# Kernel tuning notes

Measured on AMD Instinct MI355X. Metric: run time of the kernel, lower is better.

Reference implementation:

```python
import jax, jax.numpy as jnp
import numpy as np

N_NODES = 50000


def _gcn_layer(x, src, dst, norm_src, norm_dst, W, b, act):
    # DGL GraphConv with norm='both': D_out^{-1/2} A D_in^{-1/2} X W + b
    h = x * norm_src[:, None]                      # scale by src out-degree
    m = h[src]                                     # gather messages [E, d]
    agg = jax.ops.segment_sum(m, dst, num_segments=N_NODES)  # scatter-add
    agg = agg * norm_dst[:, None]
    out = agg @ W + b
    if act:
        out = jax.nn.relu(out)
    return out


def setup_inputs() -> dict:
    key = jax.random.key(0)
    ks = jax.random.split(key, 10)
    E = 800000
    in_size, hid, out_size = 128, 128, 64
    features = jax.random.normal(ks[0], (N_NODES, in_size), dtype=jnp.float32)
    src = jax.random.randint(ks[1], (E,), 0, N_NODES, dtype=jnp.int32)
    dst = jax.random.randint(ks[2], (E,), 0, N_NODES, dtype=jnp.int32)
    s = 0.05
    W1 = jax.random.normal(ks[3], (in_size, hid), dtype=jnp.float32) * s
    b1 = jnp.zeros((hid,), dtype=jnp.float32)
    W2 = jax.random.normal(ks[4], (hid, hid), dtype=jnp.float32) * s
    b2 = jnp.zeros((hid,), dtype=jnp.float32)
    W3 = jax.random.normal(ks[5], (hid, out_size), dtype=jnp.float32) * s
    b3 = jnp.zeros((out_size,), dtype=jnp.float32)
    return {"features": features, "W1": W1, "b1": b1, "W2": W2, "b2": b2,
            "W3": W3, "b3": b3, "src": src, "dst": dst}


def reference(features, W1, b1, W2, b2, W3, b3, src, dst):
    ones = jnp.ones(src.shape, dtype=features.dtype)
    out_deg = jax.ops.segment_sum(ones, src, num_segments=N_NODES)
    in_deg = jax.ops.segment_sum(ones, dst, num_segments=N_NODES)
    norm_src = jnp.maximum(out_deg, 1.0) ** -0.5   # clamp(min=1) as in DGL
    norm_dst = jnp.maximum(in_deg, 1.0) ** -0.5
    h = _gcn_layer(features, src, dst, norm_src, norm_dst, W1, b1, act=True)
    # dropout is identity in eval mode
    h = _gcn_layer(h, src, dst, norm_src, norm_dst, W2, b2, act=True)
    h = _gcn_layer(h, src, dst, norm_src, norm_dst, W3, b3, act=False)
    return h
```

## Files before the change

kernel.cpp:

```cpp
#include <hip/hip_runtime.h>
#include <math.h>

#define N_NODES 50000
#define K_DIM 128
#define CAP 64
#define CHUNK 25000
#define RH 25000
#define HWORDS 12500

typedef __attribute__((ext_vector_type(8))) short short8_t;
typedef __attribute__((ext_vector_type(4))) float f32x4_t;
typedef __attribute__((ext_vector_type(8))) _Float16 half8_t;

__device__ inline unsigned short f2bf(float x) {
    unsigned u = __float_as_uint(x);
    unsigned r = u + 0x7fffu + ((u >> 16) & 1u);
    return (unsigned short)(r >> 16);
}
__device__ inline float bf2f(unsigned short h) {
    return __uint_as_float(((unsigned)h) << 16);
}

__global__ void init_zero_kernel(_Float16* Yx, _Float16* Yy, _Float16* Yz) {
    int t = threadIdx.x;
    if (t < 128) {
        Yx[(size_t)N_NODES * 128 + t] = (_Float16)0.f;
        Yy[(size_t)N_NODES * 128 + t] = (_Float16)0.f;
    }
    if (t < 64) Yz[(size_t)N_NODES * 64 + t] = (_Float16)0.f;
}


__global__ __launch_bounds__(1024) void hist_kernel(const int* __restrict__ src,
                                                    const int* __restrict__ dst, int E,
                                                    unsigned* __restrict__ pin,
                                                    unsigned* __restrict__ pout) {
    __shared__ unsigned h[HWORDS];
    int b  = blockIdx.x >> 2;
    int io = (blockIdx.x >> 1) & 1;
    int r  = blockIdx.x & 1;
    int tid = threadIdx.x;
    for (int t = tid; t < HWORDS; t += 1024) h[t] = 0;
    __syncthreads();
    const int* keys = io ? src : dst;
    int start = b * CHUNK;
    int end = start + CHUNK; if (end > E) end = E;
    int vlo = r * RH;
    for (int i = start + tid; i < end; i += 1024) {
        int v = keys[i] - vlo;
        if ((unsigned)v < (unsigned)RH)
            atomicAdd(&h[v >> 1], 1u << ((v & 1) * 16));
    }
    __syncthreads();
    unsigned* out = io ? pout : pin;
    for (int t = tid; t < HWORDS; t += 1024)
        out[(size_t)b * (2 * HWORDS) + r * HWORDS + t] = h[t];
}

__global__ void offsets_norm_kernel(const unsigned* __restrict__ pin,
                                    const unsigned* __restrict__ pout,
                                    unsigned short* __restrict__ off16,
                                    int* __restrict__ indeg,
                                    float* __restrict__ nsrc, float* __restrict__ ndst,
                                    int n, int NB) {
    int v = blockIdx.x * blockDim.x + threadIdx.x;
    if (v >= n) return;
    int wi = v >> 1, sh = (v & 1) * 16;
    int od = 0;
    for (int b = 0; b < NB; ++b)
        od += (pout[(size_t)b * (2 * HWORDS) + wi] >> sh) & 0xffff;
    int run = 0;
    for (int b = 0; b < NB; ++b) {
        int c = (pin[(size_t)b * (2 * HWORDS) + wi] >> sh) & 0xffff;
        off16[(size_t)b * n + v] = (unsigned short)(run < CAP ? run : CAP);
        run += c;
    }
    indeg[v] = run < CAP ? run : CAP;
    int odc = od < 1 ? 1 : od;
    int idc = run < 1 ? 1 : run;
    nsrc[v] = 1.0f / sqrtf((float)odc);
    ndst[v] = 1.0f / sqrtf((float)idc);
}

__global__ __launch_bounds__(1024) void scatter_kernel(const int* __restrict__ src,
                                                       const int* __restrict__ dst, int E,
                                                       const unsigned short* __restrict__ off16,
                                                       int* __restrict__ csr, int n) {
    __shared__ unsigned cur[HWORDS];
    int b = blockIdx.x >> 1;
    int r = blockIdx.x & 1;
    int tid = threadIdx.x;
    int vlo = r * RH;
    const unsigned short* offb = off16 + (size_t)b * n + vlo;
    for (int t = tid; t < HWORDS; t += 1024)
        cur[t] = (unsigned)offb[2 * t] | ((unsigned)offb[2 * t + 1] << 16);
    __syncthreads();
    int start = b * CHUNK;
    int end = start + CHUNK; if (end > E) end = E;
    for (int i = start + tid; i < end; i += 1024) {
        int v = dst[i];
        int vr = v - vlo;
        if ((unsigned)vr < (unsigned)RH) {
            int sh = (vr & 1) * 16;
            unsigned old = atomicAdd(&cur[vr >> 1], 1u << sh);
            unsigned p = (old >> sh) & 0xffff;
            if (p < CAP) csr[((size_t)v << 6) + p] = src[i];
        }
    }
}

__global__ void split_w_all_kernel(const float* __restrict__ W1,
                                   const float* __restrict__ W2,
                                   const float* __restrict__ W3,
                                   unsigned short* __restrict__ W1h, unsigned short* __restrict__ W1l,
                                   unsigned short* __restrict__ W2h, unsigned short* __restrict__ W2l,
                                   unsigned short* __restrict__ W3h, unsigned short* __restrict__ W3l) {
    int gi = blockIdx.x * blockDim.x + threadIdx.x;
    const float* W; unsigned short *WBh, *WBl; int M, i;
    if (gi < 2048)      { W = W1; WBh = W1h; WBl = W1l; M = 128; i = gi; }
    else if (gi < 4096) { W = W2; WBh = W2h; WBl = W2l; M = 128; i = gi - 2048; }
    else if (gi < 5120) { W = W3; WBh = W3h; WBl = W3l; M = 64;  i = gi - 4096; }
    else return;
    int c    = i >> 8;
    int rem  = i & 255;
    int kc   = rem >> 6;
    int lane = rem & 63;
    int m = lane & 15, q = lane >> 4;
    int n = c * 16 + m;
    #pragma unroll
    for (int j = 0; j < 8; ++j) {
        int k = kc * 32 + q * 8 + j;
        float w = W[(size_t)k * M + n];
        unsigned short hi = f2bf(w);
        unsigned short lo = f2bf(w - bf2f(hi));
        WBh[(size_t)i * 8 + j] = hi;
        WBl[(size_t)i * 8 + j] = lo;
    }
}

template <int M>
__global__ __launch_bounds__(256) void gemm_mfma_kernel(
        const float* __restrict__ X,
        const unsigned short* __restrict__ WBh_,
        const unsigned short* __restrict__ WBl_,
        const float* __restrict__ nsrc, _Float16* __restrict__ Yh, int n) {
    constexpr int LSTR = 136;
    __shared__ short Xhi[64 * LSTR];
    __shared__ short Xlo[64 * LSTR];
    int tid = threadIdx.x;
    int lane = tid & 63, wave = tid >> 6;
    int rowBlock = blockIdx.x * 64;

    #pragma unroll
    for (int l = 0; l < 8; ++l) {
        int idx = (tid + l * 256) * 4;
        int r = idx >> 7;
        int c = idx & 127;
        float4 v = make_float4(0.f, 0.f, 0.f, 0.f);
        int gr = rowBlock + r;
        if (gr < n) v = *(const float4*)&X[(size_t)gr * K_DIM + c];
        unsigned short h0 = f2bf(v.x), h1 = f2bf(v.y), h2 = f2bf(v.z), h3 = f2bf(v.w);
        short4 hs = {(short)h0, (short)h1, (short)h2, (short)h3};
        short4 ls = {(short)f2bf(v.x - bf2f(h0)), (short)f2bf(v.y - bf2f(h1)),
                     (short)f2bf(v.z - bf2f(h2)), (short)f2bf(v.w - bf2f(h3))};
        *(short4*)&Xhi[r * LSTR + c] = hs;
        *(short4*)&Xlo[r * LSTR + c] = ls;
    }
    __syncthreads();

    int m = lane & 15, q = lane >> 4;
    short8_t ah[4], al[4];
    {
        int abase = (wave * 16 + m) * LSTR + q * 8;
        #pragma unroll
        for (int kc = 0; kc < 4; ++kc) {
            ah[kc] = *(const short8_t*)&Xhi[abase + kc * 32];
            al[kc] = *(const short8_t*)&Xlo[abase + kc * 32];
        }
    }
    float ns[4];
    int orow0 = rowBlock + wave * 16 + q * 4;
    #pragma unroll
    for (int r = 0; r < 4; ++r) ns[r] = (orow0 + r < n) ? nsrc[orow0 + r] : 0.f;

    const short8_t* WBh = (const short8_t*)WBh_;
    const short8_t* WBl = (const short8_t*)WBl_;
    constexpr int CT = M / 16;
    #pragma unroll
    for (int c = 0; c < CT; ++c) {
        short8_t bh[4], bl[4];
        #pragma unroll
        for (int kc = 0; kc < 4; ++kc) {
            bh[kc] = WBh[(c * 4 + kc) * 64 + lane];
            bl[kc] = WBl[(c * 4 + kc) * 64 + lane];
        }
        f32x4_t acc = {0.f, 0.f, 0.f, 0.f};
        #pragma unroll
        for (int kc = 0; kc < 4; ++kc) {
            acc = __builtin_amdgcn_mfma_f32_16x16x32_bf16(ah[kc], bh[kc], acc, 0, 0, 0);
            acc = __builtin_amdgcn_mfma_f32_16x16x32_bf16(ah[kc], bl[kc], acc, 0, 0, 0);
            acc = __builtin_amdgcn_mfma_f32_16x16x32_bf16(al[kc], bh[kc], acc, 0, 0, 0);
        }
        int col = c * 16 + m;
        #pragma unroll
        for (int r = 0; r < 4; ++r) {
            int row = orow0 + r;
            if (row < n) Yh[(size_t)row * M + col] = (_Float16)(acc[r] * ns[r]);
        }
    }
}

template <int MOUT>
__global__ __launch_bounds__(256) void agg_gemm_kernel(
        const _Float16* __restrict__ Yin,
        const int* __restrict__ indeg, const int* __restrict__ csr,
        const float* __restrict__ ndst, const float* __restrict__ bias,
        const unsigned short* __restrict__ WBh_,
        const unsigned short* __restrict__ WBl_,
        const float* __restrict__ nsrc, _Float16* __restrict__ Yout, int n) {
    constexpr int LSTR = 136;
    __shared__ short Xhi[64 * LSTR];
    __shared__ short Xlo[64 * LSTR];
    int tid = threadIdx.x;
    int lane = tid & 63, wave = tid >> 6;
    int rowBlock = blockIdx.x * 64;

    int sub = tid >> 4;
    int f8  = (tid & 15) * 8;
    #pragma unroll
    for (int p = 0; p < 4; ++p) {
        int r = p * 16 + sub;
        int v = rowBlock + r;
        float o[8] = {};
        if (v < n) {
            int deg = indeg[v];
            const int* __restrict__ row = &csr[(size_t)v * CAP];
            float acc[8] = {};
            for (int i = 0; i < deg; i += 4) {
                int4 ss = *(const int4*)&row[i];
                int s0 = ss.x;
                int s1 = (i + 1 < deg) ? ss.y : N_NODES;
                int s2 = (i + 2 < deg) ? ss.z : N_NODES;
                int s3 = (i + 3 < deg) ? ss.w : N_NODES;
                half8_t a = *(const half8_t*)&Yin[(size_t)s0 * 128 + f8];
                half8_t b = *(const half8_t*)&Yin[(size_t)s1 * 128 + f8];
                half8_t c = *(const half8_t*)&Yin[(size_t)s2 * 128 + f8];
                half8_t d = *(const half8_t*)&Yin[(size_t)s3 * 128 + f8];
                #pragma unroll
                for (int j = 0; j < 8; ++j)
                    acc[j] += ((float)a[j] + (float)b[j]) + ((float)c[j] + (float)d[j]);
            }
            float nd = ndst[v];
            #pragma unroll
            for (int j = 0; j < 8; ++j)
                o[j] = fmaxf(nd * acc[j] + bias[f8 + j], 0.f);
        }
        short hs[8], ls[8];
        #pragma unroll
        for (int j = 0; j < 8; ++j) {
            unsigned short h = f2bf(o[j]);
            hs[j] = (short)h;
            ls[j] = (short)f2bf(o[j] - bf2f(h));
        }
        *(short4*)&Xhi[r * LSTR + f8]     = *(short4*)&hs[0];
        *(short4*)&Xhi[r * LSTR + f8 + 4] = *(short4*)&hs[4];
        *(short4*)&Xlo[r * LSTR + f8]     = *(short4*)&ls[0];
        *(short4*)&Xlo[r * LSTR + f8 + 4] = *(short4*)&ls[4];
    }
    __syncthreads();

    int m = lane & 15, q = lane >> 4;
    short8_t ah[4], al[4];
    {
        int abase = (wave * 16 + m) * LSTR + q * 8;
        #pragma unroll
        for (int kc = 0; kc < 4; ++kc) {
            ah[kc] = *(const short8_t*)&Xhi[abase + kc * 32];
            al[kc] = *(const short8_t*)&Xlo[abase + kc * 32];
        }
    }
    float ns[4];
    int orow0 = rowBlock + wave * 16 + q * 4;
    #pragma unroll
    for (int r = 0; r < 4; ++r) ns[r] = (orow0 + r < n) ? nsrc[orow0 + r] : 0.f;

    const short8_t* WBh = (const short8_t*)WBh_;
    const short8_t* WBl = (const short8_t*)WBl_;
    constexpr int CT = MOUT / 16;
    #pragma unroll
    for (int c = 0; c < CT; ++c) {
        short8_t bh[4], bl[4];
        #pragma unroll
        for (int kc = 0; kc < 4; ++kc) {
            bh[kc] = WBh[(c * 4 + kc) * 64 + lane];
            bl[kc] = WBl[(c * 4 + kc) * 64 + lane];
        }
        f32x4_t acc = {0.f, 0.f, 0.f, 0.f};
        #pragma unroll
        for (int kc = 0; kc < 4; ++kc) {
            acc = __builtin_amdgcn_mfma_f32_16x16x32_bf16(ah[kc], bh[kc], acc, 0, 0, 0);
            acc = __builtin_amdgcn_mfma_f32_16x16x32_bf16(ah[kc], bl[kc], acc, 0, 0, 0);
            acc = __builtin_amdgcn_mfma_f32_16x16x32_bf16(al[kc], bh[kc], acc, 0, 0, 0);
        }
        int col = c * 16 + m;
        #pragma unroll
        for (int r = 0; r < 4; ++r) {
            int row = orow0 + r;
            if (row < n) Yout[(size_t)row * MOUT + col] = (_Float16)(acc[r] * ns[r]);
        }
    }
}

template <int M, bool RELU>
__global__ __launch_bounds__(256) void agg_kernel(const _Float16* __restrict__ Y,
                                                  const int* __restrict__ indeg,
                                                  const int* __restrict__ csr,
                                                  const float* __restrict__ ndst,
                                                  const float* __restrict__ bias,
                                                  float* __restrict__ Z, int n) {
    constexpr int LPN = M / 8;
    constexpr int NPB = 256 / LPN;
    int v = blockIdx.x * NPB + threadIdx.x / LPN;
    if (v >= n) return;
    int f8 = (threadIdx.x % LPN) * 8;
    int deg = indeg[v];
    const int* __restrict__ row = &csr[(size_t)v * CAP];
    float acc[8] = {};
    for (int i = 0; i < deg; i += 4) {
        int4 ss = *(const int4*)&row[i];
        int s0 = ss.x;
        int s1 = (i + 1 < deg) ? ss.y : N_NODES;
        int s2 = (i + 2 < deg) ? ss.z : N_NODES;
        int s3 = (i + 3 < deg) ? ss.w : N_NODES;
        half8_t a = *(const half8_t*)&Y[(size_t)s0 * M + f8];
        half8_t b = *(const half8_t*)&Y[(size_t)s1 * M + f8];
        half8_t c = *(const half8_t*)&Y[(size_t)s2 * M + f8];
        half8_t d = *(const half8_t*)&Y[(size_t)s3 * M + f8];
        #pragma unroll
        for (int j = 0; j < 8; ++j)
            acc[j] += ((float)a[j] + (float)b[j]) + ((float)c[j] + (float)d[j]);
    }
    float nd = ndst[v];
    float4 bb0 = *(const float4*)&bias[f8];
    float4 bb1 = *(const float4*)&bias[f8 + 4];
    float o[8];
    o[0] = nd * acc[0] + bb0.x; o[1] = nd * acc[1] + bb0.y;
    o[2] = nd * acc[2] + bb0.z; o[3] = nd * acc[3] + bb0.w;
    o[4] = nd * acc[4] + bb1.x; o[5] = nd * acc[5] + bb1.y;
    o[6] = nd * acc[6] + bb1.z; o[7] = nd * acc[7] + bb1.w;
    if (RELU) {
        #pragma unroll
        for (int j = 0; j < 8; ++j) o[j] = fmaxf(o[j], 0.f);
    }
    *(float4*)&Z[(size_t)v * M + f8]     = make_float4(o[0], o[1], o[2], o[3]);
    *(float4*)&Z[(size_t)v * M + f8 + 4] = make_float4(o[4], o[5], o[6], o[7]);
}


extern "C" void kernel_launch(void* const* d_in, const int* in_sizes, int n_in,
                              void* d_out, int out_size, void* d_ws, size_t ws_size,
                              hipStream_t stream) {
    const float* features = (const float*)d_in[0];
    const float* W1 = (const float*)d_in[1];
    const float* b1 = (const float*)d_in[2];
    const float* W2 = (const float*)d_in[3];
    const float* b2 = (const float*)d_in[4];
    const float* W3 = (const float*)d_in[5];
    const float* b3 = (const float*)d_in[6];
    const int* src = (const int*)d_in[7];
    const int* dst = (const int*)d_in[8];
    const int E = in_sizes[7];
    const int N = N_NODES;
    const int NB = (E + CHUNK - 1) / CHUNK;

    char* w = (char*)d_ws;
    auto alloc = [&](size_t bytes) {
        char* p = w;
        w += (bytes + 255) & ~(size_t)255;
        return p;
    };
    _Float16* Yx = (_Float16*)alloc((size_t)(N + 1) * 128 * 2);
    _Float16* Yy = (_Float16*)alloc((size_t)(N + 1) * 128 * 2);
    _Float16* Yz = (_Float16*)alloc((size_t)(N + 1) * 64 * 2);
    int*   csr    = (int*)alloc((size_t)N * CAP * 4);
    unsigned* pin  = (unsigned*)alloc((size_t)NB * 2 * HWORDS * 4);
    unsigned* pout = (unsigned*)alloc((size_t)NB * 2 * HWORDS * 4);
    unsigned short* off16 = (unsigned short*)alloc((size_t)NB * N * 2);
    int*   indeg  = (int*)alloc((size_t)N * 4);
    float* nsrc   = (float*)alloc((size_t)N * 4);
    float* ndst   = (float*)alloc((size_t)N * 4);
    unsigned short* W1h = (unsigned short*)alloc(128 * 128 * 2);
    unsigned short* W1l = (unsigned short*)alloc(128 * 128 * 2);
    unsigned short* W2h = (unsigned short*)alloc(128 * 128 * 2);
    unsigned short* W2l = (unsigned short*)alloc(128 * 128 * 2);
    unsigned short* W3h = (unsigned short*)alloc(64 * 128 * 2);
    unsigned short* W3l = (unsigned short*)alloc(64 * 128 * 2);

    init_zero_kernel<<<1, 128, 0, stream>>>(Yx, Yy, Yz);
    hist_kernel<<<NB * 4, 1024, 0, stream>>>(src, dst, E, pin, pout);
    offsets_norm_kernel<<<(N + 255) / 256, 256, 0, stream>>>(pin, pout, off16, indeg,
                                                             nsrc, ndst, N, NB);
    scatter_kernel<<<NB * 2, 1024, 0, stream>>>(src, dst, E, off16, csr, N);
    split_w_all_kernel<<<20, 256, 0, stream>>>(W1, W2, W3, W1h, W1l, W2h, W2l, W3h, W3l);

    int gblocks = (N + 63) / 64;
    gemm_mfma_kernel<128><<<gblocks, 256, 0, stream>>>(features, W1h, W1l, nsrc, Yx, N);
    agg_gemm_kernel<128><<<gblocks, 256, 0, stream>>>(Yx, indeg, csr, ndst, b1,
                                                      W2h, W2l, nsrc, Yy, N);
    agg_gemm_kernel<64><<<gblocks, 256, 0, stream>>>(Yy, indeg, csr, ndst, b2,
                                                     W3h, W3l, nsrc, Yz, N);
    agg_kernel<64, false><<<(N + 31) / 32, 256, 0, stream>>>(Yz, indeg, csr, ndst, b3,
                                                             (float*)d_out, N);
}
```

Baseline: 247.8 us.

## Store feature tables in 32-column chunk-major layout for cache-friendly gathers

Intermediate fp16 feature tables are rearranged from row-major [N,128] into column chunks of 32 features ([chunk][N+1][32]). The aggregation kernels now loop over chunks, so each pass gathers from a 3.2 MB slice that fits better in L2/MALL, and each row is handled by 4 threads instead of 16. The cost is that the CSR row indices are re-read once per chunk, and per-node parallelism within a block drops, which could lengthen the serial latency chains on nodes with high degree.

```diff
diff --git a/kernel.cpp b/kernel.cpp
--- a/kernel.cpp
+++ b/kernel.cpp
@@ -8,6 +8,8 @@
 #define RH 25000
 #define HWORDS 12500
 
+#define CSP ((size_t)(N_NODES + 1) * 32)
+
 typedef __attribute__((ext_vector_type(8))) short short8_t;
 typedef __attribute__((ext_vector_type(4))) float f32x4_t;
 typedef __attribute__((ext_vector_type(8))) _Float16 half8_t;
@@ -23,11 +25,10 @@
 
 __global__ void init_zero_kernel(_Float16* Yx, _Float16* Yy, _Float16* Yz) {
     int t = threadIdx.x;
-    if (t < 128) {
-        Yx[(size_t)N_NODES * 128 + t] = (_Float16)0.f;
-        Yy[(size_t)N_NODES * 128 + t] = (_Float16)0.f;
-    }
-    if (t < 64) Yz[(size_t)N_NODES * 64 + t] = (_Float16)0.f;
+    int c = t >> 5, f = t & 31;
+    Yx[c * CSP + (size_t)N_NODES * 32 + f] = (_Float16)0.f;
+    Yy[c * CSP + (size_t)N_NODES * 32 + f] = (_Float16)0.f;
+    if (c < 2) Yz[c * CSP + (size_t)N_NODES * 32 + f] = (_Float16)0.f;
 }
 
 
@@ -202,10 +203,12 @@
             acc = __builtin_amdgcn_mfma_f32_16x16x32_bf16(al[kc], bh[kc], acc, 0, 0, 0);
         }
         int col = c * 16 + m;
+        int ch = col >> 5, cc = col & 31;
         #pragma unroll
         for (int r = 0; r < 4; ++r) {
             int row = orow0 + r;
-            if (row < n) Yh[(size_t)row * M + col] = (_Float16)(acc[r] * ns[r]);
+            if (row < n)
+                Yh[(size_t)ch * CSP + (size_t)row * 32 + cc] = (_Float16)(acc[r] * ns[r]);
         }
     }
 }
@@ -225,16 +228,17 @@
     int lane = tid & 63, wave = tid >> 6;
     int rowBlock = blockIdx.x * 64;
 
-    int sub = tid >> 4;
-    int f8  = (tid & 15) * 8;
-    #pragma unroll
-    for (int p = 0; p < 4; ++p) {
-        int r = p * 16 + sub;
+    {
+        int r  = tid >> 2;
+        int j  = tid & 3;
+        int f8 = j * 8;
         int v = rowBlock + r;
-        float o[8] = {};
-        if (v < n) {
-            int deg = indeg[v];
-            const int* __restrict__ row = &csr[(size_t)v * CAP];
+        int deg = 0; float nd = 0.f;
+        const int* __restrict__ row = &csr[(size_t)v * CAP];
+        if (v < n) { deg = indeg[v]; nd = ndst[v]; }
+        #pragma unroll 1
+        for (int cch = 0; cch < 4; ++cch) {
+            const _Float16* __restrict__ base = Yin + (size_t)cch * CSP + f8;
             float acc[8] = {};
             for (int i = 0; i < deg; i += 4) {
                 int4 ss = *(const int4*)&row[i];
@@ -242,30 +246,32 @@
                 int s1 = (i + 1 < deg) ? ss.y : N_NODES;
                 int s2 = (i + 2 < deg) ? ss.z : N_NODES;
                 int s3 = (i + 3 < deg) ? ss.w : N_NODES;
-                half8_t a = *(const half8_t*)&Yin[(size_t)s0 * 128 + f8];
-                half8_t b = *(const half8_t*)&Yin[(size_t)s1 * 128 + f8];
-                half8_t c = *(const half8_t*)&Yin[(size_t)s2 * 128 + f8];
-                half8_t d = *(const half8_t*)&Yin[(size_t)s3 * 128 + f8];
+                half8_t a  = *(const half8_t*)&base[(size_t)s0 * 32];
+                half8_t b  = *(const half8_t*)&base[(size_t)s1 * 32];
+                half8_t c2 = *(const half8_t*)&base[(size_t)s2 * 32];
+                half8_t d  = *(const half8_t*)&base[(size_t)s3 * 32];
                 #pragma unroll
-                for (int j = 0; j < 8; ++j)
-                    acc[j] += ((float)a[j] + (float)b[j]) + ((float)c[j] + (float)d[j]);
+                for (int t = 0; t < 8; ++t)
+                    acc[t] += ((float)a[t] + (float)b[t]) + ((float)c2[t] + (float)d[t]);
             }
-            float nd = ndst[v];
+            float o[8] = {};
+            if (v < n) {
+                #pragma unroll
+                for (int t = 0; t < 8; ++t)
+                    o[t] = fmaxf(nd * acc[t] + bias[cch * 32 + f8 + t], 0.f);
+            }
+            short hs[8], ls[8];
             #pragma unroll
-            for (int j = 0; j < 8; ++j)
-                o[j] = fmaxf(nd * acc[j] + bias[f8 + j], 0.f);
-        }
-        short hs[8], ls[8];
-        #pragma unroll
-        for (int j = 0; j < 8; ++j) {
-            unsigned short h = f2bf(o[j]);
-            hs[j] = (short)h;
-            ls[j] = (short)f2bf(o[j] - bf2f(h));
-        }
-        *(short4*)&Xhi[r * LSTR + f8]     = *(short4*)&hs[0];
-        *(short4*)&Xhi[r * LSTR + f8 + 4] = *(short4*)&hs[4];
-        *(short4*)&Xlo[r * LSTR + f8]     = *(short4*)&ls[0];
-        *(short4*)&Xlo[r * LSTR + f8 + 4] = *(short4*)&ls[4];
+            for (int t = 0; t < 8; ++t) {
+                unsigned short h = f2bf(o[t]);
+                hs[t] = (short)h;
+                ls[t] = (short)f2bf(o[t] - bf2f(h));
+            }
+            *(short4*)&Xhi[r * LSTR + cch * 32 + f8]     = *(short4*)&hs[0];
+            *(short4*)&Xhi[r * LSTR + cch * 32 + f8 + 4] = *(short4*)&hs[4];
+            *(short4*)&Xlo[r * LSTR + cch * 32 + f8]     = *(short4*)&ls[0];
+            *(short4*)&Xlo[r * LSTR + cch * 32 + f8 + 4] = *(short4*)&ls[4];
+        }
     }
     __syncthreads();
 
@@ -303,57 +309,59 @@
             acc = __builtin_amdgcn_mfma_f32_16x16x32_bf16(al[kc], bh[kc], acc, 0, 0, 0);
         }
         int col = c * 16 + m;
+        int ch = col >> 5, cc = col & 31;
         #pragma unroll
         for (int r = 0; r < 4; ++r) {
             int row = orow0 + r;
-            if (row < n) Yout[(size_t)row * MOUT + col] = (_Float16)(acc[r] * ns[r]);
-        }
-    }
-}
-
-template <int M, bool RELU>
-__global__ __launch_bounds__(256) void agg_kernel(const _Float16* __restrict__ Y,
-                                                  const int* __restrict__ indeg,
-                                                  const int* __restrict__ csr,
-                                                  const float* __restrict__ ndst,
-                                                  const float* __restrict__ bias,
-                                                  float* __restrict__ Z, int n) {
-    constexpr int LPN = M / 8;
-    constexpr int NPB = 256 / LPN;
-    int v = blockIdx.x * NPB + threadIdx.x / LPN;
+            if (row < n)
+                Yout[(size_t)ch * CSP + (size_t)row * 32 + cc] = (_Float16)(acc[r] * ns[r]);
+        }
+    }
+}
+
+__global__ __launch_bounds__(256) void agg_final_kernel(const _Float16* __restrict__ Y,
+                                                        const int* __restrict__ indeg,
+                                                        const int* __restrict__ csr,
+                                                        const float* __restrict__ ndst,
+                                                        const float* __restrict__ bias,
+                                                        float* __restrict__ Z, int n) {
+    int r = threadIdx.x >> 2;
+    int j = threadIdx.x & 3;
+    int f8 = j * 8;
+    int v = blockIdx.x * 64 + r;
     if (v >= n) return;
-    int f8 = (threadIdx.x % LPN) * 8;
     int deg = indeg[v];
+    float nd = ndst[v];
     const int* __restrict__ row = &csr[(size_t)v * CAP];
-    float acc[8] = {};
-    for (int i = 0; i < deg; i += 4) {
-        int4 ss = *(const int4*)&row[i];
-        int s0 = ss.x;
-        int s1 = (i + 1 < deg) ? ss.y : N_NODES;
-        int s2 = (i + 2 < deg) ? ss.z : N_NODES;
-        int s3 = (i + 3 < deg) ? ss.w : N_NODES;
-        half8_t a = *(const half8_t*)&Y[(size_t)s0 * M + f8];
-        half8_t b = *(const half8_t*)&Y[(size_t)s1 * M + f8];
-        half8_t c = *(const half8_t*)&Y[(size_t)s2 * M + f8];
-        half8_t d = *(const half8_t*)&Y[(size_t)s3 * M + f8];
-        #pragma unroll
-        for (int j = 0; j < 8; ++j)
-            acc[j] += ((float)a[j] + (float)b[j]) + ((float)c[j] + (float)d[j]);
-    }
-    float nd = ndst[v];
-    float4 bb0 = *(const float4*)&bias[f8];
-    float4 bb1 = *(const float4*)&bias[f8 + 4];
-    float o[8];
-    o[0] = nd * acc[0] + bb0.x; o[1] = nd * acc[1] + bb0.y;
-    o[2] = nd * acc[2] + bb0.z; o[3] = nd * acc[3] + bb0.w;
-    o[4] = nd * acc[4] + bb1.x; o[5] = nd * acc[5] + bb1.y;
-    o[6] = nd * acc[6] + bb1.z; o[7] = nd * acc[7] + bb1.w;
-    if (RELU) {
-        #pragma unroll
-        for (int j = 0; j < 8; ++j) o[j] = fmaxf(o[j], 0.f);
-    }
-    *(float4*)&Z[(size_t)v * M + f8]     = make_float4(o[0], o[1], o[2], o[3]);
-    *(float4*)&Z[(size_t)v * M + f8 + 4] = make_float4(o[4], o[5], o[6], o[7]);
+    #pragma unroll 1
+    for (int c = 0; c < 2; ++c) {
+        const _Float16* __restrict__ base = Y + (size_t)c * CSP + f8;
+        float acc[8] = {};
+        for (int i = 0; i < deg; i += 4) {
+            int4 ss = *(const int4*)&row[i];
+            int s0 = ss.x;
+            int s1 = (i + 1 < deg) ? ss.y : N_NODES;
+            int s2 = (i + 2 < deg) ? ss.z : N_NODES;
+            int s3 = (i + 3 < deg) ? ss.w : N_NODES;
+            half8_t a  = *(const half8_t*)&base[(size_t)s0 * 32];
+            half8_t b  = *(const half8_t*)&base[(size_t)s1 * 32];
+            half8_t c2 = *(const half8_t*)&base[(size_t)s2 * 32];
+            half8_t d  = *(const half8_t*)&base[(size_t)s3 * 32];
+            #pragma unroll
+            for (int t = 0; t < 8; ++t)
+                acc[t] += ((float)a[t] + (float)b[t]) + ((float)c2[t] + (float)d[t]);
+        }
+        int f = c * 32 + f8;
+        float4 bb0 = *(const float4*)&bias[f];
+        float4 bb1 = *(const float4*)&bias[f + 4];
+        float o[8];
+        o[0] = nd * acc[0] + bb0.x; o[1] = nd * acc[1] + bb0.y;
+        o[2] = nd * acc[2] + bb0.z; o[3] = nd * acc[3] + bb0.w;
+        o[4] = nd * acc[4] + bb1.x; o[5] = nd * acc[5] + bb1.y;
+        o[6] = nd * acc[6] + bb1.z; o[7] = nd * acc[7] + bb1.w;
+        *(float4*)&Z[(size_t)v * 64 + f]     = make_float4(o[0], o[1], o[2], o[3]);
+        *(float4*)&Z[(size_t)v * 64 + f + 4] = make_float4(o[4], o[5], o[6], o[7]);
+    }
 }
 
 
@@ -409,6 +417,6 @@
                                                       W2h, W2l, nsrc, Yy, N);
     agg_gemm_kernel<64><<<gblocks, 256, 0, stream>>>(Yy, indeg, csr, ndst, b2,
                                                      W3h, W3l, nsrc, Yz, N);
-    agg_kernel<64, false><<<(N + 31) / 32, 256, 0, stream>>>(Yz, indeg, csr, ndst, b3,
-                                                             (float*)d_out, N);
-}
+    agg_final_kernel<<<gblocks, 256, 0, stream>>>(Yz, indeg, csr, ndst, b3,
+                                                  (float*)d_out, N);
+}
```

Measured after the change: 261.9 us. +5.7%, slower.

## Halve agg_gemm row tile and unroll gather loops to eight neighbors

Applied to the files above, without the earlier changes.

The fused aggregate+GEMM kernel now handles 32 rows per block instead of 64. The four waves split the output as two row tiles by two column halves, which doubles the grid and halves shared memory per block. Both gather loops fetch eight neighbor rows per iteration instead of four, putting more loads in flight to hide gather latency. The cost is more register pressure and wasted padded loads for nodes whose degree is not a multiple of eight, and each wave now reads the weight tile for only half the columns.

```diff
diff --git a/kernel.cpp b/kernel.cpp
--- a/kernel.cpp
+++ b/kernel.cpp
@@ -219,16 +219,16 @@
         const unsigned short* __restrict__ WBl_,
         const float* __restrict__ nsrc, _Float16* __restrict__ Yout, int n) {
     constexpr int LSTR = 136;
-    __shared__ short Xhi[64 * LSTR];
-    __shared__ short Xlo[64 * LSTR];
+    __shared__ short Xhi[32 * LSTR];
+    __shared__ short Xlo[32 * LSTR];
     int tid = threadIdx.x;
     int lane = tid & 63, wave = tid >> 6;
-    int rowBlock = blockIdx.x * 64;
+    int rowBlock = blockIdx.x * 32;
 
     int sub = tid >> 4;
     int f8  = (tid & 15) * 8;
     #pragma unroll
-    for (int p = 0; p < 4; ++p) {
+    for (int p = 0; p < 2; ++p) {
         int r = p * 16 + sub;
         int v = rowBlock + r;
         float o[8] = {};
@@ -236,19 +236,29 @@
             int deg = indeg[v];
             const int* __restrict__ row = &csr[(size_t)v * CAP];
             float acc[8] = {};
-            for (int i = 0; i < deg; i += 4) {
-                int4 ss = *(const int4*)&row[i];
-                int s0 = ss.x;
-                int s1 = (i + 1 < deg) ? ss.y : N_NODES;
-                int s2 = (i + 2 < deg) ? ss.z : N_NODES;
-                int s3 = (i + 3 < deg) ? ss.w : N_NODES;
+            for (int i = 0; i < deg; i += 8) {
+                int4 sa = *(const int4*)&row[i];
+                int4 sb = *(const int4*)&row[i + 4];
+                int s0 = sa.x;
+                int s1 = (i + 1 < deg) ? sa.y : N_NODES;
+                int s2 = (i + 2 < deg) ? sa.z : N_NODES;
+                int s3 = (i + 3 < deg) ? sa.w : N_NODES;
+                int s4 = (i + 4 < deg) ? sb.x : N_NODES;
+                int s5 = (i + 5 < deg) ? sb.y : N_NODES;
+                int s6 = (i + 6 < deg) ? sb.z : N_NODES;
+                int s7 = (i + 7 < deg) ? sb.w : N_NODES;
                 half8_t a = *(const half8_t*)&Yin[(size_t)s0 * 128 + f8];
                 half8_t b = *(const half8_t*)&Yin[(size_t)s1 * 128 + f8];
                 half8_t c = *(const half8_t*)&Yin[(size_t)s2 * 128 + f8];
                 half8_t d = *(const half8_t*)&Yin[(size_t)s3 * 128 + f8];
+                half8_t e = *(const half8_t*)&Yin[(size_t)s4 * 128 + f8];
+                half8_t f = *(const half8_t*)&Yin[(size_t)s5 * 128 + f8];
+                half8_t g = *(const half8_t*)&Yin[(size_t)s6 * 128 + f8];
+                half8_t h = *(const half8_t*)&Yin[(size_t)s7 * 128 + f8];
                 #pragma unroll
                 for (int j = 0; j < 8; ++j)
-                    acc[j] += ((float)a[j] + (float)b[j]) + ((float)c[j] + (float)d[j]);
+                    acc[j] += (((float)a[j] + (float)b[j]) + ((float)c[j] + (float)d[j]))
+                            + (((float)e[j] + (float)f[j]) + ((float)g[j] + (float)h[j]));
             }
             float nd = ndst[v];
             #pragma unroll
@@ -270,9 +280,11 @@
     __syncthreads();
 
     int m = lane & 15, q = lane >> 4;
+    int wrow = wave & 1;
+    int wcol = wave >> 1;
     short8_t ah[4], al[4];
     {
-        int abase = (wave * 16 + m) * LSTR + q * 8;
+        int abase = (wrow * 16 + m) * LSTR + q * 8;
         #pragma unroll
         for (int kc = 0; kc < 4; ++kc) {
             ah[kc] = *(const short8_t*)&Xhi[abase + kc * 32];
@@ -280,15 +292,16 @@
         }
     }
     float ns[4];
-    int orow0 = rowBlock + wave * 16 + q * 4;
+    int orow0 = rowBlock + wrow * 16 + q * 4;
     #pragma unroll
     for (int r = 0; r < 4; ++r) ns[r] = (orow0 + r < n) ? nsrc[orow0 + r] : 0.f;
 
     const short8_t* WBh = (const short8_t*)WBh_;
     const short8_t* WBl = (const short8_t*)WBl_;
-    constexpr int CT = MOUT / 16;
-    #pragma unroll
-    for (int c = 0; c < CT; ++c) {
+    constexpr int CTH = MOUT / 32;
+    #pragma unroll
+    for (int c2 = 0; c2 < CTH; ++c2) {
+        int c = wcol * CTH + c2;
         short8_t bh[4], bl[4];
         #pragma unroll
         for (int kc = 0; kc < 4; ++kc) {
@@ -326,19 +339,29 @@
     int deg = indeg[v];
     const int* __restrict__ row = &csr[(size_t)v * CAP];
     float acc[8] = {};
-    for (int i = 0; i < deg; i += 4) {
-        int4 ss = *(const int4*)&row[i];
-        int s0 = ss.x;
-        int s1 = (i + 1 < deg) ? ss.y : N_NODES;
-        int s2 = (i + 2 < deg) ? ss.z : N_NODES;
-        int s3 = (i + 3 < deg) ? ss.w : N_NODES;
+    for (int i = 0; i < deg; i += 8) {
+        int4 sa = *(const int4*)&row[i];
+        int4 sb = *(const int4*)&row[i + 4];
+        int s0 = sa.x;
+        int s1 = (i + 1 < deg) ? sa.y : N_NODES;
+        int s2 = (i + 2 < deg) ? sa.z : N_NODES;
+        int s3 = (i + 3 < deg) ? sa.w : N_NODES;
+        int s4 = (i + 4 < deg) ? sb.x : N_NODES;
+        int s5 = (i + 5 < deg) ? sb.y : N_NODES;
+        int s6 = (i + 6 < deg) ? sb.z : N_NODES;
+        int s7 = (i + 7 < deg) ? sb.w : N_NODES;
         half8_t a = *(const half8_t*)&Y[(size_t)s0 * M + f8];
         half8_t b = *(const half8_t*)&Y[(size_t)s1 * M + f8];
         half8_t c = *(const half8_t*)&Y[(size_t)s2 * M + f8];
         half8_t d = *(const half8_t*)&Y[(size_t)s3 * M + f8];
+        half8_t e = *(const half8_t*)&Y[(size_t)s4 * M + f8];
+        half8_t f = *(const half8_t*)&Y[(size_t)s5 * M + f8];
+        half8_t g = *(const half8_t*)&Y[(size_t)s6 * M + f8];
+        half8_t h = *(const half8_t*)&Y[(size_t)s7 * M + f8];
         #pragma unroll
         for (int j = 0; j < 8; ++j)
-            acc[j] += ((float)a[j] + (float)b[j]) + ((float)c[j] + (float)d[j]);
+            acc[j] += (((float)a[j] + (float)b[j]) + ((float)c[j] + (float)d[j]))
+                    + (((float)e[j] + (float)f[j]) + ((float)g[j] + (float)h[j]));
     }
     float nd = ndst[v];
     float4 bb0 = *(const float4*)&bias[f8];
@@ -403,12 +426,13 @@
     scatter_kernel<<<NB * 2, 1024, 0, stream>>>(src, dst, E, off16, csr, N);
     split_w_all_kernel<<<20, 256, 0, stream>>>(W1, W2, W3, W1h, W1l, W2h, W2l, W3h, W3l);
 
-    int gblocks = (N + 63) / 64;
-    gemm_mfma_kernel<128><<<gblocks, 256, 0, stream>>>(features, W1h, W1l, nsrc, Yx, N);
-    agg_gemm_kernel<128><<<gblocks, 256, 0, stream>>>(Yx, indeg, csr, ndst, b1,
-                                                      W2h, W2l, nsrc, Yy, N);
-    agg_gemm_kernel<64><<<gblocks, 256, 0, stream>>>(Yy, indeg, csr, ndst, b2,
-                                                     W3h, W3l, nsrc, Yz, N);
+    int gblocks64 = (N + 63) / 64;
+    int gblocks32 = (N + 31) / 32;
+    gemm_mfma_kernel<128><<<gblocks64, 256, 0, stream>>>(features, W1h, W1l, nsrc, Yx, N);
+    agg_gemm_kernel<128><<<gblocks32, 256, 0, stream>>>(Yx, indeg, csr, ndst, b1,
+                                                        W2h, W2l, nsrc, Yy, N);
+    agg_gemm_kernel<64><<<gblocks32, 256, 0, stream>>>(Yy, indeg, csr, ndst, b2,
+                                                       W3h, W3l, nsrc, Yz, N);
     agg_kernel<64, false><<<(N + 31) / 32, 256, 0, stream>>>(Yz, indeg, csr, ndst, b3,
                                                              (float*)d_out, N);
 }
```

After: 240.2 us. 1.03x faster.
